# Kernel tuning notes

Hardware: AMD Instinct MI355X
Metric: run time of the kernel (lower is better)

Reference implementation:

```python
import jax, jax.numpy as jnp
import numpy as np

NEG_BIG = -9e15

def setup_inputs() -> dict:
    key = jax.random.key(0)
    k1, k2, k3, k4, k5 = jax.random.split(key, 5)
    N, IN, OUT = 10000, 128, 64
    h = jax.random.normal(k1, (N, IN), dtype=jnp.float32)
    adj = jax.random.randint(k2, (N, N), 0, 2, dtype=jnp.int32)
    W = jax.random.normal(k3, (IN, OUT), dtype=jnp.float32) * 0.1
    a1 = jax.random.normal(k4, (OUT, 1), dtype=jnp.float32) * 0.1
    a2 = jax.random.normal(k5, (OUT, 1), dtype=jnp.float32) * 0.1
    return {"h": h, "adj": adj, "W": W, "a1": a1, "a2": a2}

def reference(h, adj, W, a1, a2):
    alpha = 0.2  # LeakyReLU negative slope
    Wh = h @ W                      # [N, OUT] (dropout off: eval mode)
    # NOTE: original code adds two [N,1] vectors -> e stays [N,1] (per-row score)
    e = Wh @ a1 + Wh @ a2           # [N, 1]
    e = jnp.where(e > 0, e, alpha * e)
    # broadcast [N,1] score against [N,N] adjacency mask
    scores = jnp.where(adj > 0, e, NEG_BIG)   # [N, N]
    attention = jax.nn.softmax(scores, axis=1)
    h_prime = attention @ Wh        # [N, OUT]
    return h_prime
```

## Files before the change

### kernel.cpp

```cpp
#include <hip/hip_runtime.h>


#define N_NODES 10000
#define KPAD    10016
#define NSTEP   313
#define OUTF    64

typedef __attribute__((ext_vector_type(8))) short short8;
typedef __attribute__((ext_vector_type(4))) float f32x4;

__device__ __forceinline__ unsigned short f2bf(float x) {
    unsigned int u = __builtin_bit_cast(unsigned int, x);
    u = (u + 0x7FFFu + ((u >> 16) & 1u)) >> 16;
    return (unsigned short)u;
}

__global__ __launch_bounds__(256) void wh_pack_kernel(
    const float* __restrict__ h, const float* __restrict__ W,
    unsigned short* __restrict__ Bpack) {
    __shared__ float Wl[128 * 64];
    __shared__ float Hl[16 * 128];
    const int tid = threadIdx.x;
    const int i0  = blockIdx.x * 16;
    const float4* W4 = (const float4*)W;
    float4* Wl4 = (float4*)Wl;
    #pragma unroll
    for (int t = 0; t < 8; ++t) Wl4[t * 256 + tid] = W4[t * 256 + tid];
    const float4* H4 = (const float4*)(h + (size_t)i0 * 128);
    float4* Hl4 = (float4*)Hl;
    #pragma unroll
    for (int t = 0; t < 2; ++t) Hl4[t * 256 + tid] = H4[t * 256 + tid];
    if (blockIdx.x == 0) {
        #pragma unroll
        for (int t = 0; t < 4; ++t)
            Bpack[(size_t)N_NODES * OUTF + tid * 4 + t] = 0;
    }
    __syncthreads();
    const int n  = tid & 63;
    const int rq = tid >> 6;
    float acc0 = 0.f, acc1 = 0.f, acc2 = 0.f, acc3 = 0.f;
    #pragma unroll 8
    for (int j = 0; j < 128; ++j) {
        const float w = Wl[j * 64 + n];
        acc0 += Hl[(rq * 4 + 0) * 128 + j] * w;
        acc1 += Hl[(rq * 4 + 1) * 128 + j] * w;
        acc2 += Hl[(rq * 4 + 2) * 128 + j] * w;
        acc3 += Hl[(rq * 4 + 3) * 128 + j] * w;
    }
    const float accs[4] = {acc0, acc1, acc2, acc3};
    #pragma unroll
    for (int t = 0; t < 4; ++t) {
        const int i = i0 + rq * 4 + t;
        Bpack[((size_t)(i >> 3) * 64 + n) * 8 + (i & 7)] = f2bf(accs[t]);
    }
}

__global__ __launch_bounds__(256) void gat_agg_kernel(
    const int* __restrict__ adj, const unsigned short* __restrict__ Bpack,
    float* __restrict__ Cpart, int* __restrict__ degpart, int S) {
    const int bx   = blockIdx.x;
    const int tile = bx / S;
    const int q    = bx - tile * S;
    const int tidx = threadIdx.x;
    const int wave = tidx >> 6;
    const int lane = tidx & 63;
    const int r16  = lane & 15;
    const int quad = lane >> 4;
    const int row  = tile * 16 + r16;
    const int* __restrict__ arow = adj + (size_t)row * N_NODES;
    const short8* __restrict__ bbase = (const short8*)Bpack;

    f32x4 acc[4];
    #pragma unroll
    for (int c = 0; c < 4; ++c) acc[c] = (f32x4){0.f, 0.f, 0.f, 0.f};
    int msum = 0;

    const int slot = q * 4 + wave;
    const int stride = S * 4;
    for (int s = slot; s < NSTEP; s += stride) {
        const int k0 = s * 32;
        const int kq = k0 + quad * 8;
        short8 afrag;
        if (k0 + 32 <= N_NODES) {
            const int4 v0 = *(const int4*)(arow + kq);
            const int4 v1 = *(const int4*)(arow + kq + 4);
            const int vs[8] = {v0.x, v0.y, v0.z, v0.w, v1.x, v1.y, v1.z, v1.w};
            #pragma unroll
            for (int t = 0; t < 8; ++t) {
                const int m = vs[t] > 0;
                afrag[t] = m ? (short)0x3F80 : (short)0;
                msum += m;
            }
        } else {
            #pragma unroll
            for (int t = 0; t < 8; ++t) {
                const int k = kq + t;
                const int v = (k < N_NODES) ? arow[k] : 0;
                const int m = v > 0;
                afrag[t] = m ? (short)0x3F80 : (short)0;
                msum += m;
            }
        }
        const int g = (k0 >> 3) + quad;
        const short8* __restrict__ bg = bbase + (size_t)g * 64 + r16;
        const short8 b0 = bg[0];
        const short8 b1 = bg[16];
        const short8 b2 = bg[32];
        const short8 b3 = bg[48];
        acc[0] = __builtin_amdgcn_mfma_f32_16x16x32_bf16(afrag, b0, acc[0], 0, 0, 0);
        acc[1] = __builtin_amdgcn_mfma_f32_16x16x32_bf16(afrag, b1, acc[1], 0, 0, 0);
        acc[2] = __builtin_amdgcn_mfma_f32_16x16x32_bf16(afrag, b2, acc[2], 0, 0, 0);
        acc[3] = __builtin_amdgcn_mfma_f32_16x16x32_bf16(afrag, b3, acc[3], 0, 0, 0);
    }

    msum += __shfl_down(msum, 32);
    msum += __shfl_down(msum, 16);

    __shared__ float Cred[4][16][64];
    __shared__ int   degred[4][16];
    #pragma unroll
    for (int c = 0; c < 4; ++c) {
        #pragma unroll
        for (int r = 0; r < 4; ++r)
            Cred[wave][quad * 4 + r][c * 16 + r16] = acc[c][r];
    }
    if (lane < 16) degred[wave][lane] = msum;
    __syncthreads();

    for (int e = tidx; e < 16 * 64; e += 256) {
        const int r = e >> 6, n = e & 63;
        const float sum = Cred[0][r][n] + Cred[1][r][n] + Cred[2][r][n] + Cred[3][r][n];
        Cpart[((size_t)q * N_NODES + tile * 16 + r) * 64 + n] = sum;
    }
    if (tidx < 16)
        degpart[q * N_NODES + tile * 16 + tidx] =
            degred[0][tidx] + degred[1][tidx] + degred[2][tidx] + degred[3][tidx];
}

__global__ __launch_bounds__(256) void finalize_kernel(
    const float* __restrict__ Cpart, const int* __restrict__ degpart,
    float* __restrict__ out, int S) {
    const int idx = blockIdx.x * 256 + threadIdx.x;
    if (idx >= N_NODES * OUTF) return;
    const int i = idx >> 6;
    float sum = 0.f;
    int deg = 0;
    for (int qq = 0; qq < S; ++qq) {
        sum += Cpart[(size_t)qq * N_NODES * OUTF + idx];
        deg += degpart[qq * N_NODES + i];
    }
    out[idx] = (deg > 0) ? sum / (float)deg : 0.f;
}

extern "C" void kernel_launch(void* const* d_in, const int* in_sizes, int n_in,
                              void* d_out, int out_size, void* d_ws, size_t ws_size,
                              hipStream_t stream) {
    const float* h   = (const float*)d_in[0];
    const int*   adj = (const int*)d_in[1];
    const float* W   = (const float*)d_in[2];
    float* out = (float*)d_out;
    char*  ws  = (char*)d_ws;

    const size_t bpack_bytes = (size_t)KPAD * OUTF * 2;
    const size_t off = (bpack_bytes + 255) & ~(size_t)255;

    int S = 8;
    while (S > 1) {
        const size_t need = off + (size_t)S * N_NODES * OUTF * 4
                                + (size_t)S * N_NODES * 4;
        if (need <= ws_size) break;
        S >>= 1;
    }

    unsigned short* Bpack = (unsigned short*)ws;
    float* Cpart;
    int*   degpart;
    if (S == 1 && off + (size_t)N_NODES * OUTF * 4 + (size_t)N_NODES * 4 > ws_size) {
        Cpart   = out;
        degpart = (int*)(ws + off);
    } else {
        Cpart   = (float*)(ws + off);
        degpart = (int*)(ws + off + (size_t)S * N_NODES * OUTF * 4);
    }

    wh_pack_kernel<<<dim3(625), dim3(256), 0, stream>>>(h, W, Bpack);
    gat_agg_kernel<<<dim3(625 * S), dim3(256), 0, stream>>>(adj, Bpack, Cpart, degpart, S);
    finalize_kernel<<<dim3((N_NODES * OUTF + 255) / 256), dim3(256), 0, stream>>>(
        Cpart, degpart, out, S);
}
```

Measured before the change: 566.9 us.

## Pre-pack adjacency into a bitmask before the MFMA aggregation pass

Adds a kernel that streams the int32 adjacency matrix once and compresses it to one bit per edge in a per-row bitmask. The aggregation kernel then reads 32-bit mask words instead of 32 bytes of ints per lane per step, and builds the bf16 A-fragment and degree count from bits with popc. The aim is to move the dominant 400MB read into a simple, highly parallel streaming kernel with many independent loads, instead of the latency-bound gather inside the MFMA loop. The trade-offs are an extra launch, a mask round-trip through memory, and the removal of the workspace-size fallback: S is now fixed at 8 regardless of how much workspace is available.

```diff
diff --git a/kernel.cpp b/kernel.cpp
--- a/kernel.cpp
+++ b/kernel.cpp
@@ -5,6 +5,7 @@
 #define KPAD    10016
 #define NSTEP   313
 #define OUTF    64
+#define MROWB   1280
 
 typedef __attribute__((ext_vector_type(8))) short short8;
 typedef __attribute__((ext_vector_type(4))) float f32x4;
@@ -55,8 +56,39 @@
     }
 }
 
+__global__ __launch_bounds__(256) void mask_pack_kernel(
+    const int* __restrict__ adj, unsigned int* __restrict__ mask) {
+    const int row = blockIdx.x;
+    const int tid = threadIdx.x;
+    const int4* __restrict__ arow4 = (const int4*)(adj + (size_t)row * N_NODES);
+    unsigned int* __restrict__ mrow = mask + (size_t)row * (MROWB / 4);
+    for (int w = tid; w < MROWB / 4; w += 256) {
+        unsigned int word = 0u;
+        if (w < 312) {
+            #pragma unroll
+            for (int j = 0; j < 8; ++j) {
+                const int4 v = arow4[w * 8 + j];
+                word |= (v.x != 0 ? 1u : 0u) << (j * 4 + 0);
+                word |= (v.y != 0 ? 1u : 0u) << (j * 4 + 1);
+                word |= (v.z != 0 ? 1u : 0u) << (j * 4 + 2);
+                word |= (v.w != 0 ? 1u : 0u) << (j * 4 + 3);
+            }
+        } else if (w == 312) {
+            #pragma unroll
+            for (int j = 0; j < 4; ++j) {
+                const int4 v = arow4[w * 8 + j];
+                word |= (v.x != 0 ? 1u : 0u) << (j * 4 + 0);
+                word |= (v.y != 0 ? 1u : 0u) << (j * 4 + 1);
+                word |= (v.z != 0 ? 1u : 0u) << (j * 4 + 2);
+                word |= (v.w != 0 ? 1u : 0u) << (j * 4 + 3);
+            }
+        }
+        mrow[w] = word;
+    }
+}
+
 __global__ __launch_bounds__(256) void gat_agg_kernel(
-    const int* __restrict__ adj, const unsigned short* __restrict__ Bpack,
+    const unsigned int* __restrict__ mask, const unsigned short* __restrict__ Bpack,
     float* __restrict__ Cpart, int* __restrict__ degpart, int S) {
     const int bx   = blockIdx.x;
     const int tile = bx / S;
@@ -67,7 +99,7 @@
     const int r16  = lane & 15;
     const int quad = lane >> 4;
     const int row  = tile * 16 + r16;
-    const int* __restrict__ arow = adj + (size_t)row * N_NODES;
+    const unsigned int* __restrict__ mrow = mask + (size_t)row * (MROWB / 4);
     const short8* __restrict__ bbase = (const short8*)Bpack;
 
     f32x4 acc[4];
@@ -78,30 +110,14 @@
     const int slot = q * 4 + wave;
     const int stride = S * 4;
     for (int s = slot; s < NSTEP; s += stride) {
-        const int k0 = s * 32;
-        const int kq = k0 + quad * 8;
+        const unsigned int m   = mrow[s];
+        const unsigned int myb = (m >> (quad * 8)) & 0xFFu;
         short8 afrag;
-        if (k0 + 32 <= N_NODES) {
-            const int4 v0 = *(const int4*)(arow + kq);
-            const int4 v1 = *(const int4*)(arow + kq + 4);
-            const int vs[8] = {v0.x, v0.y, v0.z, v0.w, v1.x, v1.y, v1.z, v1.w};
-            #pragma unroll
-            for (int t = 0; t < 8; ++t) {
-                const int m = vs[t] > 0;
-                afrag[t] = m ? (short)0x3F80 : (short)0;
-                msum += m;
-            }
-        } else {
-            #pragma unroll
-            for (int t = 0; t < 8; ++t) {
-                const int k = kq + t;
-                const int v = (k < N_NODES) ? arow[k] : 0;
-                const int m = v > 0;
-                afrag[t] = m ? (short)0x3F80 : (short)0;
-                msum += m;
-            }
-        }
-        const int g = (k0 >> 3) + quad;
+        #pragma unroll
+        for (int t = 0; t < 8; ++t)
+            afrag[t] = ((myb >> t) & 1u) ? (short)0x3F80 : (short)0;
+        msum += (int)__popc(myb);
+        const int g = s * 4 + quad;
         const short8* __restrict__ bg = bbase + (size_t)g * 64 + r16;
         const short8 b0 = bg[0];
         const short8 b1 = bg[16];
@@ -160,31 +176,20 @@
     const float* W   = (const float*)d_in[2];
     float* out = (float*)d_out;
     char*  ws  = (char*)d_ws;
+    const int S = 8;
 
-    const size_t bpack_bytes = (size_t)KPAD * OUTF * 2;
-    const size_t off = (bpack_bytes + 255) & ~(size_t)255;
-
-    int S = 8;
-    while (S > 1) {
-        const size_t need = off + (size_t)S * N_NODES * OUTF * 4
-                                + (size_t)S * N_NODES * 4;
-        if (need <= ws_size) break;
-        S >>= 1;
-    }
-
-    unsigned short* Bpack = (unsigned short*)ws;
-    float* Cpart;
-    int*   degpart;
-    if (S == 1 && off + (size_t)N_NODES * OUTF * 4 + (size_t)N_NODES * 4 > ws_size) {
-        Cpart   = out;
-        degpart = (int*)(ws + off);
-    } else {
-        Cpart   = (float*)(ws + off);
-        degpart = (int*)(ws + off + (size_t)S * N_NODES * OUTF * 4);
-    }
+    size_t off = 0;
+    unsigned short* Bpack = (unsigned short*)(ws + off);
+    off += ((size_t)KPAD * OUTF * 2 + 255) & ~(size_t)255;
+    unsigned int* mask = (unsigned int*)(ws + off);
+    off += ((size_t)N_NODES * MROWB + 255) & ~(size_t)255;
+    int* degpart = (int*)(ws + off);
+    off += ((size_t)S * N_NODES * 4 + 255) & ~(size_t)255;
+    float* Cpart = (float*)(ws + off);
 
     wh_pack_kernel<<<dim3(625), dim3(256), 0, stream>>>(h, W, Bpack);
-    gat_agg_kernel<<<dim3(625 * S), dim3(256), 0, stream>>>(adj, Bpack, Cpart, degpart, S);
+    mask_pack_kernel<<<dim3(N_NODES), dim3(256), 0, stream>>>(adj, mask);
+    gat_agg_kernel<<<dim3(625 * S), dim3(256), 0, stream>>>(mask, Bpack, Cpart, degpart, S);
     finalize_kernel<<<dim3((N_NODES * OUTF + 255) / 256), dim3(256), 0, stream>>>(
         Cpart, degpart, out, S);
 }
```

Result: slower. 593.7 us (+4.7%).
